# Optimization experiments

Measured on AMD Instinct MI355X. Metric: run time of the kernel, lower is better.

## Reference

```python
import jax, jax.numpy as jnp
import numpy as np

NTRIAL, NNEUR, NT, NT_FULL, NTAU, NLAT, NPAD = 8, 100, 256, 300, 50, 8, 44
LR, JITTER, ZERO_THRESH = 0.2, 1e-3, 1e-5


def setup_inputs() -> dict:
    key = jax.random.key(0)
    k1, k2, k3, k4 = jax.random.split(key, 4)
    Y = jax.random.uniform(k1, (NTRIAL, NNEUR, NT), dtype=jnp.float32)
    raw_input = jax.random.uniform(k2, (NTRIAL, NNEUR, NT_FULL), dtype=jnp.float32)
    kernel = 0.05 * jax.random.normal(k3, (NNEUR, NTAU, NNEUR), dtype=jnp.float32)
    readout = 0.02 * jax.random.normal(k4, (NNEUR, NLAT), dtype=jnp.float32)
    t = jnp.arange(NT, dtype=jnp.float32)
    K = jnp.exp(-(t[:, None] - t[None, :]) ** 2 / (2.0 * 20.0 ** 2))  # RBF latent covariance
    bias = jnp.zeros((), jnp.float32)
    return {"Y": Y, "raw_input": raw_input, "kernel": kernel, "readout": readout,
            "K": K, "bias": bias, "max_iter": 5}


def _conv(raw_input, kernel, npadding):
    # raw_input: (m, i, nt_full); kernel: (i, ntau, j)
    ntrial, ni, nt = raw_input.shape
    zero_pad = jnp.zeros((kernel.shape[0], 1, kernel.shape[2]), kernel.dtype)
    kernel = jnp.concatenate([zero_pad, kernel], axis=1)  # enforce causality
    ntau = kernel.shape[1]
    nn = nt + ntau - 1
    Fx = jnp.fft.fft(raw_input, n=nn, axis=2)[:, :, :, None]   # (m, i, nn, 1)
    Fk = jnp.fft.fft(kernel, n=nn, axis=1)[None]                # (1, i, nn, j)
    G = jnp.fft.ifft(Fx * Fk, axis=2).real
    G = jnp.where(jnp.abs(G) < ZERO_THRESH, 0.0, G)
    G = G[:, :, npadding:nt, :]                                 # (m, i, t, j)
    return jnp.transpose(G, (0, 1, 3, 2)).astype(raw_input.dtype)  # (m, i, j, t)


def _gpfa_poisson_fix_weights(Y, weights, K, bias, max_iter):
    # Y: (m, n, t); weights: (m, n, l, t); K: (t, t)
    ntrial, nneuron, nlatent, nt = weights.shape
    I = jnp.eye(nt, dtype=K.dtype)
    inv_K = jnp.linalg.inv(K + JITTER * I)
    w2 = weights ** 2
    mu0 = jnp.zeros((ntrial, nlatent, nt), K.dtype)
    hess0 = jnp.broadcast_to(inv_K, (ntrial, nlatent, nt, nt)) + jnp.zeros((ntrial, nlatent, 1, 1), K.dtype)

    def step(carry, _):
        mu, hessian, _, _ = carry
        log_lambd = jnp.einsum('mnlt,mlt->mnt', weights, mu) + bias
        hinv = jnp.linalg.inv(hessian)                              # (m, l, t, t)
        dhinv = jnp.diagonal(hinv, axis1=-2, axis2=-1)              # (m, l, t)
        lambd = jnp.exp(log_lambd + 0.5 * jnp.einsum('mlt,mnlt->mnt', dhinv, w2))
        iKh = jnp.einsum('tu,mluv->mltv', inv_K, hinv)              # inv_K @ hessian^{-1}
        muK = jnp.einsum('mlt,tu->mlu', mu, inv_K)
        _, logabs = jnp.linalg.slogdet(iKh)
        loss = (jnp.sum(Y * log_lambd) - jnp.sum(lambd)
                - 0.5 * jnp.sum(muK * mu)
                - 0.5 * jnp.sum(jnp.trace(iKh, axis1=-2, axis2=-1))
                + 0.5 * jnp.sum(logabs) - nt)
        grad = jnp.einsum('mnlt,mnt->mlt', weights, Y - lambd) - muK
        w2l = jnp.einsum('mnlt,mnt->mlt', w2, lambd)                # (m, l, t)
        new_h = -inv_K[None, None] - w2l[..., None] * I             # 4D diagonal add
        mu_upd = jnp.linalg.solve(new_h, grad[..., None])[..., 0]
        return (mu - LR * mu_upd, new_h, lambd, loss), None

    carry0 = (mu0, hess0, jnp.zeros_like(Y), jnp.zeros((), K.dtype))
    (mu, hessian, lambd, loss), _ = jax.lax.scan(step, carry0, None, length=max_iter)
    return mu, lambd, loss


def reference(Y, raw_input, kernel, readout, K, bias, max_iter):
    G = _conv(raw_input, kernel, NPAD)                       # (m, i, j, t)
    weights = jnp.einsum('mijt,il->mjlt', G, readout)        # (m, n=j, l, t)
    mu, lambd, loss = _gpfa_poisson_fix_weights(Y, weights, K, bias, max_iter)
    return mu, lambd, loss
```

## Files before the change

kernel.cpp:

```cpp
#include <hip/hip_runtime.h>

#define NTRIAL 8
#define NNEUR 100
#define NTT 256
#define NT_FULL 300
#define NTAU 50
#define NLAT 8
#define NPAD 44
#define LRATE 0.2f
#define JITTER 0.001f
#define NMAT 64
#define NSLOT 136
#define SPITCH 260
#define NBLKF 35360
#define NBLKF4 8840

__device__ __forceinline__ int bslot(int I, int J){ return ((I*(I+1))>>1) + J; }
__device__ __forceinline__ int eidx(int I, int J, int i, int j){
    return bslot(I,J)*SPITCH + i*16 + ((((j>>2) + (i>>2))&3)<<2) + (j&3);
}
__device__ __forceinline__ int f4idx(int I, int J, int i, int q){
    return bslot(I,J)*65 + i*4 + ((q + (i>>2))&3);
}
__device__ __forceinline__ int bsidx(int J, int k, int col){
    return J*260 + k*16 + ((((col>>2) + (k>>2))&3)<<2) + (col&3);
}
#define DOT4(u,v) (u.x*v.x + u.y*v.y + u.z*v.z + u.w*v.w)

__device__ __forceinline__ void gemm16(const float4* P4, int baseA, int baseB,
                                       int ti, int tj, float acc[4][4]){
    #pragma unroll
    for (int kc = 0; kc < 4; ++kc){
        float4 a0 = P4[baseA + (ti+0)*4 + ((kc + ((ti+0)>>2))&3)];
        float4 a1 = P4[baseA + (ti+1)*4 + ((kc + ((ti+1)>>2))&3)];
        float4 a2 = P4[baseA + (ti+2)*4 + ((kc + ((ti+2)>>2))&3)];
        float4 a3 = P4[baseA + (ti+3)*4 + ((kc + ((ti+3)>>2))&3)];
        float4 b0 = P4[baseB + (tj+0)*4 + ((kc + ((tj+0)>>2))&3)];
        float4 b1 = P4[baseB + (tj+1)*4 + ((kc + ((tj+1)>>2))&3)];
        float4 b2 = P4[baseB + (tj+2)*4 + ((kc + ((tj+2)>>2))&3)];
        float4 b3 = P4[baseB + (tj+3)*4 + ((kc + ((tj+3)>>2))&3)];
        acc[0][0]+=DOT4(a0,b0); acc[0][1]+=DOT4(a0,b1); acc[0][2]+=DOT4(a0,b2); acc[0][3]+=DOT4(a0,b3);
        acc[1][0]+=DOT4(a1,b0); acc[1][1]+=DOT4(a1,b1); acc[1][2]+=DOT4(a1,b2); acc[1][3]+=DOT4(a1,b3);
        acc[2][0]+=DOT4(a2,b0); acc[2][1]+=DOT4(a2,b1); acc[2][2]+=DOT4(a2,b2); acc[2][3]+=DOT4(a2,b3);
        acc[3][0]+=DOT4(a3,b0); acc[3][1]+=DOT4(a3,b1); acc[3][2]+=DOT4(a3,b2); acc[3][3]+=DOT4(a3,b3);
    }
}

__global__ void k_zero(float* mu, float* scal){
    int i = blockIdx.x*256 + threadIdx.x;
    if (i < 16384) mu[i] = 0.f;
    if (i < 64) scal[i] = 0.f;
}

__global__ void k_transpose(const float* __restrict__ kern, float* __restrict__ kt){
    int idx = blockIdx.x*256 + threadIdx.x;
    if (idx >= NNEUR*NTAU*NNEUR) return;
    int i = idx/(NTAU*NNEUR); int rem = idx%(NTAU*NNEUR);
    int tau = rem/NNEUR; int j = rem%NNEUR;
    kt[((size_t)i*NNEUR + j)*NTAU + tau] = kern[idx];
}

__global__ __launch_bounds__(256) void k_conv_weights(const float* __restrict__ raw,
                                                      const float* __restrict__ kt,
                                                      const float* __restrict__ readout,
                                                      float* __restrict__ W){
    int b = blockIdx.x; int m = b / NNEUR; int j = b % NNEUR; int t = threadIdx.x;
    __shared__ float ro[NNEUR*NLAT];
    __shared__ float raw_s[10][NT_FULL];
    __shared__ float kern_s[10][NTAU];
    for (int idx = t; idx < NNEUR*NLAT; idx += 256) ro[idx] = readout[idx];
    float acc[NLAT];
    #pragma unroll
    for (int l = 0; l < NLAT; ++l) acc[l] = 0.f;
    int tmax = min(NTAU, t + NPAD);
    for (int c = 0; c < 10; ++c){
        __syncthreads();
        for (int idx = t; idx < 10*NT_FULL; idx += 256){
            int ii = idx / NT_FULL, tt = idx % NT_FULL;
            raw_s[ii][tt] = raw[((size_t)m*NNEUR + c*10 + ii)*NT_FULL + tt];
        }
        for (int idx = t; idx < 10*NTAU; idx += 256){
            int ii = idx / NTAU, tau = idx % NTAU;
            kern_s[ii][tau] = kt[((size_t)(c*10 + ii)*NNEUR + j)*NTAU + tau];
        }
        __syncthreads();
        for (int ii = 0; ii < 10; ++ii){
            float g = 0.f;
            const float* kr = kern_s[ii];
            const float* rr = raw_s[ii];
            for (int tau = 1; tau <= tmax; ++tau) g += kr[tau-1] * rr[t + NPAD - tau];
            if (fabsf(g) < 1e-5f) g = 0.f;
            const float* rop = &ro[(c*10 + ii)*NLAT];
            #pragma unroll
            for (int l = 0; l < NLAT; ++l) acc[l] += rop[l]*g;
        }
    }
    #pragma unroll
    for (int l = 0; l < NLAT; ++l) W[(((size_t)b)*NLAT + l)*NTT + t] = acc[l];
}

template<int MODE>
__global__ __launch_bounds__(512) void k_fact(
    const float* __restrict__ Kin,
    const float* __restrict__ invKb,
    const float* __restrict__ W,
    const float* __restrict__ Y,
    const float* __restrict__ bias_p,
    const float* __restrict__ muIn,
    const float* __restrict__ diagIn,
    float* __restrict__ muOut,
    float* __restrict__ diagOut,
    float* __restrict__ lambd,
    float* __restrict__ Sout,
    float* __restrict__ scal,
    int it0, int it4, int itSlot)
{
    __shared__ float4 P4[NBLKF4];
    __shared__ float4 Bs4[1040];
    __shared__ float dlog[256];
    __shared__ float idg[16];
    __shared__ float extra[1024];
    float* P    = (float*)P4;
    float* Bsf  = (float*)Bs4;
    float* gs   = extra;
    float* w2ls = extra + 256;
    float* red  = extra + 512;
    float* muown = dlog;
    const int t = threadIdx.x;
    const int b = blockIdx.x;
    const int g = t>>4, gt = t&15;
    const int ti = (gt>>2)<<2, tj = (gt&3)<<2;
    const int lanebase = t & 48;

    if (MODE == 0){
        if (t < 256){
            int r = t, I = r>>4, i = r&15;
            for (int c = 0; c <= r; ++c)
                P[eidx(I, c>>4, i, c&15)] = Kin[r*256 + c] + ((c==r)?JITTER:0.f);
        }
        __syncthreads();
    } else {
        const int m_ = b >> 3, l_ = b & 7;
        const float4* G4 = (const float4*)invKb;
        for (int e = t; e < NBLKF4; e += 512) P4[e] = G4[e];
        const int t2 = t & 255, half = t >> 8;
        float mul[NLAT], dhl[NLAT];
        #pragma unroll
        for (int l = 0; l < NLAT; ++l){
            mul[l] = muIn[((size_t)(m_*NLAT + l))*NTT + t2];
            dhl[l] = it0 ? (1.0f + JITTER) : (-diagIn[((size_t)(m_*NLAT + l))*NTT + t2]);
        }
        if (t < 256) muown[t] = mul[l_];
        float bias = bias_p[0];
        float gacc = 0.f, w2acc = 0.f, yl = 0.f, ls = 0.f;
        for (int n = half*50; n < half*50 + 50; ++n){
            size_t base = (((size_t)(m_*NNEUR + n))*NLAT)*NTT + t2;
            float wl[NLAT];
            float ll = bias, q = 0.f;
            #pragma unroll
            for (int l = 0; l < NLAT; ++l){
                float w = W[base + (size_t)l*NTT];
                wl[l] = w;
                ll += w * mul[l];
                q  += w * w * dhl[l];
            }
            float lam = expf(ll + 0.5f*q);
            float yv = Y[((size_t)(m_*NNEUR + n))*NTT + t2];
            float wo = wl[l_];
            gacc  += wo * (yv - lam);
            w2acc += wo * wo * lam;
            if (it4){
                lambd[((size_t)(m_*NNEUR + n))*NTT + t2] = lam;
                yl += yv * ll; ls += lam;
            }
        }
        Bsf[half*256 + t2]       = gacc;
        Bsf[512 + half*256 + t2] = w2acc;
        __syncthreads();
        if (it4){
            red[t] = yl;
            __syncthreads();
            for (int s = 256; s > 0; s >>= 1){ if (t < s) red[t] += red[t+s]; __syncthreads(); }
            if (t == 0 && l_ == 0) atomicAdd(&scal[0], red[0]);
            __syncthreads();
            red[t] = ls;
            __syncthreads();
            for (int s = 256; s > 0; s >>= 1){ if (t < s) red[t] += red[t+s]; __syncthreads(); }
            if (t == 0 && l_ == 0) atomicAdd(&scal[1], red[0]);
            __syncthreads();
        }
        if (t < 256){
            float gg = Bsf[t] + Bsf[256 + t];
            float w2 = Bsf[512 + t] + Bsf[768 + t];
            int T = t>>4, tb = t&15;
            float mk = 0.f;
            for (int U = 0; U < 16; ++U){
                if (U <= T){
                    #pragma unroll
                    for (int u = 0; u < 16; ++u) mk += muown[U*16+u] * P[eidx(T,U,tb,u)];
                } else {
                    #pragma unroll
                    for (int u = 0; u < 16; ++u) mk += muown[U*16+u] * P[eidx(U,T,u,tb)];
                }
            }
            gs[t]   = gg - mk;
            w2ls[t] = w2;
            red[t]  = mk * muown[t];
        } else red[t] = 0.f;
        if (it4){
            __syncthreads();
            for (int s = 256; s > 0; s >>= 1){ if (t < s) red[t] += red[t+s]; __syncthreads(); }
            if (t == 0) atomicAdd(&scal[2], red[0]);
        }
        __syncthreads();
        if (t < 256) P[eidx(t>>4, t>>4, t&15, t&15)] += w2ls[t];
        __syncthreads();
    }

    for (int p = 0; p < 16; ++p){
        const int pm = p - 1;
        if (g == 31){
            float x[16];
            if (p > 0){
                float acc[4][4];
                #pragma unroll
                for (int aa=0;aa<4;++aa){acc[aa][0]=0;acc[aa][1]=0;acc[aa][2]=0;acc[aa][3]=0;}
                gemm16(P4, bslot(p,pm)*65, bslot(p,pm)*65, ti, tj, acc);
                #pragma unroll
                for (int aa = 0; aa < 4; ++aa){
                    int oi = f4idx(p,p,ti+aa,tj>>2);
                    float4 c = P4[oi];
                    c.x-=acc[aa][0]; c.y-=acc[aa][1]; c.z-=acc[aa][2]; c.w-=acc[aa][3];
                    P4[oi] = c;
                }
            }
            #pragma unroll
            for (int q = 0; q < 4; ++q){
                float4 v = P4[f4idx(p,p,gt,q)];
                x[4*q]=v.x; x[4*q+1]=v.y; x[4*q+2]=v.z; x[4*q+3]=v.w;
            }
            const int i = gt;
            #pragma unroll
            for (int k = 0; k < 16; ++k){
                float piv = __shfl(x[k], lanebase + k, 64);
                float d = sqrtf(piv);
                float dinv = 1.f/d;
                float lik = (i == k) ? d : x[k]*dinv;
                if (i >= k) x[k] = lik;
                #pragma unroll
                for (int c = k+1; c < 16; ++c){
                    float lck = __shfl(x[k], lanebase + c, 64);
                    if (i >= c) x[c] -= lik*lck;
                }
                if (i == k){ idg[k] = dinv; dlog[p*16+k] = d; }
            }
            #pragma unroll
            for (int q = 0; q < 4; ++q)
                P4[f4idx(p,p,i,q)] = make_float4(x[4*q],x[4*q+1],x[4*q+2],x[4*q+3]);
        } else if (p > 0 && g < 28){
            int m = 16 - p;
            int npairs = (m*(m+1))>>1;
            for (int q = 1+g; q < npairs; q += 28){
                int di = (int)floorf((sqrtf(8.f*(float)q + 1.f) - 1.f)*0.5f);
                while (((di+1)*(di+2))>>1 <= q) ++di;
                while ((di*(di+1))>>1 > q) --di;
                int dj = q - ((di*(di+1))>>1);
                int I = p+di, J = p+dj;
                float acc[4][4];
                #pragma unroll
                for (int aa=0;aa<4;++aa){acc[aa][0]=0;acc[aa][1]=0;acc[aa][2]=0;acc[aa][3]=0;}
                gemm16(P4, bslot(I,pm)*65, bslot(J,pm)*65, ti, tj, acc);
                #pragma unroll
                for (int aa = 0; aa < 4; ++aa){
                    int oi = f4idx(I,J,ti+aa,tj>>2);
                    float4 c = P4[oi];
                    c.x-=acc[aa][0]; c.y-=acc[aa][1]; c.z-=acc[aa][2]; c.w-=acc[aa][3];
                    P4[oi] = c;
                }
            }
        }
        __syncthreads();
        if (p < 15){
            int nrows = (15 - p)*16;
            if (t < nrows){
                int r = (p+1)*16 + t;
                int I = r>>4, i = r&15;
                float x[16];
                #pragma unroll
                for (int q = 0; q < 4; ++q){
                    float4 v = P4[f4idx(I,p,i,q)];
                    x[4*q]=v.x; x[4*q+1]=v.y; x[4*q+2]=v.z; x[4*q+3]=v.w;
                }
                #pragma unroll
                for (int c = 0; c < 16; ++c){
                    float s = x[c];
                    #pragma unroll
                    for (int j = 0; j < c; ++j) s -= x[j]*P[eidx(p,p,c,j)];
                    x[c] = s*idg[c];
                }
                #pragma unroll
                for (int q = 0; q < 4; ++q)
                    P4[f4idx(I,p,i,q)] = make_float4(x[4*q],x[4*q+1],x[4*q+2],x[4*q+3]);
            }
        }
        __syncthreads();
    }

    for (int I = 0; I < 16; ++I){
        if (g == 31){
            const int j = gt;
            float col[16];
            #pragma unroll
            for (int k=0;k<16;++k) col[k] = 0.f;
            #pragma unroll
            for (int i = 0; i < 16; ++i){
                float Lii = P[eidx(I,I,i,i)];
                float s = 0.f;
                #pragma unroll
                for (int k = 0; k < 16; ++k){
                    if (k < i){ float term = P[eidx(I,I,i,k)]*col[k]; s += (k >= j) ? term : 0.f; }
                }
                col[i] = (i == j) ? (1.f/Lii) : ((i > j) ? (-s/Lii) : 0.f);
            }
            #pragma unroll
            for (int q = 0; q < 4; ++q)
                P4[f4idx(I,I,j,q)] = make_float4(col[4*q],col[4*q+1],col[4*q+2],col[4*q+3]);
        } else {
            int pj = g>>1, half = g&1;
            if (pj < I){
                const int J = pj;
                float acc[4][4];
                #pragma unroll
                for (int aa=0;aa<4;++aa){acc[aa][0]=0;acc[aa][1]=0;acc[aa][2]=0;acc[aa][3]=0;}
                for (int K = J+half; K < I; K += 2)
                    gemm16(P4, bslot(I,K)*65, bslot(K,J)*65, ti, tj, acc);
                #pragma unroll
                for (int aa = 0; aa < 4; ++aa){
                    #pragma unroll
                    for (int bb = 0; bb < 4; ++bb)
                        acc[aa][bb] += __shfl_xor(acc[aa][bb], 16, 64);
                }
                if (half == 0){
                    #pragma unroll
                    for (int aa = 0; aa < 4; ++aa)
                        Bs4[J*65 + (ti+aa)*4 + (((tj>>2)+((ti+aa)>>2))&3)] =
                            make_float4(acc[aa][0],acc[aa][1],acc[aa][2],acc[aa][3]);
                }
            }
        }
        __syncthreads();
        {
            int pj = g>>1;
            if (pj < I && g < 31){
                const int J = pj;
                const int u = ((g&1)<<4) | gt;
                const int ti2 = ((u>>3)&3)<<2;
                const int tjb = (u&7)<<1;
                float acc2[4][2];
                acc2[0][0]=0;acc2[0][1]=0;acc2[1][0]=0;acc2[1][1]=0;
                acc2[2][0]=0;acc2[2][1]=0;acc2[3][0]=0;acc2[3][1]=0;
                #pragma unroll
                for (int k = 0; k < 16; ++k){
                    float4 sa = P4[f4idx(I,I,k,ti2>>2)];
                    float b0 = Bsf[bsidx(J,k,tjb)];
                    float b1 = Bsf[bsidx(J,k,tjb+1)];
                    acc2[0][0]+=sa.x*b0; acc2[0][1]+=sa.x*b1;
                    acc2[1][0]+=sa.y*b0; acc2[1][1]+=sa.y*b1;
                    acc2[2][0]+=sa.z*b0; acc2[2][1]+=sa.z*b1;
                    acc2[3][0]+=sa.w*b0; acc2[3][1]+=sa.w*b1;
                }
                #pragma unroll
                for (int bb = 0; bb < 2; ++bb)
                    P4[f4idx(I,J,tjb+bb,ti2>>2)] =
                        make_float4(-acc2[0][bb],-acc2[1][bb],-acc2[2][bb],-acc2[3][bb]);
            }
        }
        __syncthreads();
    }

    if (MODE == 0){
        red[t] = (t < 256) ? 2.f*logf(dlog[t]) : 0.f;
        __syncthreads();
        for (int s = 256; s > 0; s >>= 1){ if (t < s) red[t] += red[t+s]; __syncthreads(); }
        if (t == 0) scal[20] = red[0];
        float4* SO = (float4*)Sout;
        for (int e = t; e < NBLKF4; e += 512) SO[e] = P4[e];
        return;
    } else {
        float* zp = Bsf;
        float dsum = 0.f;
        if (t < 256){
            const int J0 = t>>4, j0 = t&15;
            for (int I = J0; I < 16; ++I){
                #pragma unroll
                for (int q = 0; q < 4; ++q){
                    float4 v = P4[f4idx(I,J0,j0,q)];
                    dsum += v.x*v.x + v.y*v.y + v.z*v.z + v.w*v.w;
                }
            }
            diagOut[b*256 + t] = dsum;
            const int Ir = t>>4, rb = t&15;
            float z = 0.f;
            for (int J = 0; J <= Ir; ++J){
                #pragma unroll
                for (int j = 0; j < 16; ++j) z += P[eidx(Ir,J,j,rb)]*gs[J*16+j];
            }
            zp[t] = z;
        }
        __syncthreads();
        if (t < 256){
            const int J0 = t>>4, j0 = t&15;
            float u = 0.f;
            for (int I = J0; I < 16; ++I){
                #pragma unroll
                for (int q = 0; q < 4; ++q){
                    float4 v = P4[f4idx(I,J0,j0,q)];
                    const float* zz = &zp[I*16 + 4*q];
                    u += v.x*zz[0] + v.y*zz[1] + v.z*zz[2] + v.w*zz[3];
                }
            }
            muOut[b*256 + t] = muIn[b*256 + t] + LRATE*u;
            red[t]       = w2ls[t]*dsum;
            red[256 + t] = 2.f*logf(dlog[t]);
        }
        __syncthreads();
        for (int s = 128; s > 0; s >>= 1){
            if (t < s){ red[t] += red[t+s]; red[256+t] += red[256+t+s]; }
            __syncthreads();
        }
        if (t == 0){
            atomicAdd(&scal[8 + itSlot],  red[0] - 256.f);
            atomicAdd(&scal[24 + itSlot], -scal[20] - red[256]);
        }
    }
}

__global__ __launch_bounds__(256) void k_syrk(const float* __restrict__ S,
                                              float* __restrict__ invKb){
    int sidx = blockIdx.x;
    int I = (int)floorf((sqrtf(8.f*(float)sidx + 1.f) - 1.f)*0.5f);
    while (((I+1)*(I+2))>>1 <= sidx) ++I;
    while ((I*(I+1))>>1 > sidx) --I;
    int J = sidx - ((I*(I+1))>>1);
    int t = threadIdx.x; int i = t>>4, j = t&15;
    __shared__ float4 sA[64], sB[64];
    const float4* S4 = (const float4*)S;
    float s = 0.f;
    for (int R = I; R < 16; ++R){
        __syncthreads();
        if (t < 64) sA[t] = S4[bslot(R,I)*65 + t];
        else if (t < 128) sB[t-64] = S4[bslot(R,J)*65 + t-64];
        __syncthreads();
        #pragma unroll
        for (int q = 0; q < 4; ++q){
            float4 a = sA[i*4 + ((q + (i>>2))&3)];
            float4 c = sB[j*4 + ((q + (j>>2))&3)];
            s += a.x*c.x + a.y*c.y + a.z*c.z + a.w*c.w;
        }
    }
    invKb[eidx(I,J,i,j)] = s;
}

__global__ void k_loss(const float* __restrict__ scal, float* __restrict__ out_loss){
    out_loss[0] = scal[0] - scal[1] - 0.5f*scal[2] - 0.5f*scal[8+3] + 0.5f*scal[24+3] - 256.f;
}

__global__ void k_gather(const float* __restrict__ mu, const float* __restrict__ lambd, float* __restrict__ out){
    int idx = blockIdx.x*256 + threadIdx.x;
    if (idx < 16384) out[idx] = mu[idx];
    else if (idx < 16384 + 204800) out[idx] = lambd[idx - 16384];
}

extern "C" void kernel_launch(void* const* d_in, const int* in_sizes, int n_in,
                              void* d_out, int out_size, void* d_ws, size_t ws_size,
                              hipStream_t stream){
    (void)in_sizes; (void)n_in; (void)out_size; (void)ws_size;
    const float* Y       = (const float*)d_in[0];
    const float* raw     = (const float*)d_in[1];
    const float* kern    = (const float*)d_in[2];
    const float* readout = (const float*)d_in[3];
    const float* K       = (const float*)d_in[4];
    const float* bias    = (const float*)d_in[5];
    float* out = (float*)d_out;
    float* ws  = (float*)d_ws;

    float* invKb  = ws;
    float* Sblk   = invKb + NBLKF;
    float* W      = Sblk + NBLKF;
    float* muA    = W + 1638400;
    float* muB    = muA + 16384;
    float* lambd  = muB + 16384;
    float* diagA  = lambd + 204800;
    float* diagB  = diagA + 16384;
    float* scal   = diagB + 16384;
    float* kt     = scal + 64;

    k_zero<<<64, 256, 0, stream>>>(muA, scal);
    k_transpose<<<(NNEUR*NTAU*NNEUR + 255)/256, 256, 0, stream>>>(kern, kt);
    k_conv_weights<<<NTRIAL*NNEUR, 256, 0, stream>>>(raw, kt, readout, W);

    k_fact<0><<<1, 512, 0, stream>>>(K, nullptr, nullptr, nullptr, nullptr, nullptr, nullptr,
                                     nullptr, nullptr, nullptr, Sblk, scal, 0, 0, 0);
    k_syrk<<<NSLOT, 256, 0, stream>>>(Sblk, invKb);

    for (int it = 0; it < 5; ++it){
        const float* muI = (it & 1) ? muB : muA;
        float*       muO = (it & 1) ? muA : muB;
        const float* dI  = (it & 1) ? diagB : diagA;
        float*       dO  = (it & 1) ? diagA : diagB;
        k_fact<1><<<NMAT, 512, 0, stream>>>(nullptr, invKb, W, Y, bias, muI, dI,
                                            muO, dO, lambd, nullptr, scal,
                                            (it == 0) ? 1 : 0, (it == 4) ? 1 : 0, it);
    }
    k_loss<<<1, 1, 0, stream>>>(scal, out + 16384 + 204800);
    k_gather<<<864, 256, 0, stream>>>(muB, lambd, out);
}
```

Before: 1.537 ms.

## Split gradient into separate kernel and fuse Cholesky inversion into factorization loop

Moves the Poisson rate/gradient computation out of the factorization kernel into a new k_grad2 kernel. Each block of k_grad2 handles a slice of neurons and produces all 8 latents for one trial, so W is read once per trial instead of eight times. The blocked Cholesky is also restructured so each diagonal block is inverted right after it is factored. The panel solve and the L-inverse off-diagonal products become small GEMMs against the inverted diagonal block, interleaved in one pass instead of a separate second sweep. This adds a kernel launch and global partial buffers per iteration, and changes the accumulation order.

```diff
diff --git a/kernel.cpp b/kernel.cpp
--- a/kernel.cpp
+++ b/kernel.cpp
@@ -16,29 +16,30 @@
 #define NBLKF4 8840
 
 __device__ __forceinline__ int bslot(int I, int J){ return ((I*(I+1))>>1) + J; }
+__device__ __forceinline__ int rcs(int i, int j){
+    return i*16 + ((((j>>2) + (i>>2))&3)<<2) + (j&3);
+}
 __device__ __forceinline__ int eidx(int I, int J, int i, int j){
-    return bslot(I,J)*SPITCH + i*16 + ((((j>>2) + (i>>2))&3)<<2) + (j&3);
-}
+    return bslot(I,J)*SPITCH + rcs(i,j);
+}
+__device__ __forceinline__ int rc4(int i, int q){ return i*4 + ((q + (i>>2))&3); }
 __device__ __forceinline__ int f4idx(int I, int J, int i, int q){
-    return bslot(I,J)*65 + i*4 + ((q + (i>>2))&3);
-}
-__device__ __forceinline__ int bsidx(int J, int k, int col){
-    return J*260 + k*16 + ((((col>>2) + (k>>2))&3)<<2) + (col&3);
+    return bslot(I,J)*65 + rc4(i,q);
 }
 #define DOT4(u,v) (u.x*v.x + u.y*v.y + u.z*v.z + u.w*v.w)
 
-__device__ __forceinline__ void gemm16(const float4* P4, int baseA, int baseB,
+__device__ __forceinline__ void gemmRR(const float4* A, int baseA, const float4* B, int baseB,
                                        int ti, int tj, float acc[4][4]){
     #pragma unroll
     for (int kc = 0; kc < 4; ++kc){
-        float4 a0 = P4[baseA + (ti+0)*4 + ((kc + ((ti+0)>>2))&3)];
-        float4 a1 = P4[baseA + (ti+1)*4 + ((kc + ((ti+1)>>2))&3)];
-        float4 a2 = P4[baseA + (ti+2)*4 + ((kc + ((ti+2)>>2))&3)];
-        float4 a3 = P4[baseA + (ti+3)*4 + ((kc + ((ti+3)>>2))&3)];
-        float4 b0 = P4[baseB + (tj+0)*4 + ((kc + ((tj+0)>>2))&3)];
-        float4 b1 = P4[baseB + (tj+1)*4 + ((kc + ((tj+1)>>2))&3)];
-        float4 b2 = P4[baseB + (tj+2)*4 + ((kc + ((tj+2)>>2))&3)];
-        float4 b3 = P4[baseB + (tj+3)*4 + ((kc + ((tj+3)>>2))&3)];
+        float4 a0 = A[baseA + rc4(ti+0,kc)];
+        float4 a1 = A[baseA + rc4(ti+1,kc)];
+        float4 a2 = A[baseA + rc4(ti+2,kc)];
+        float4 a3 = A[baseA + rc4(ti+3,kc)];
+        float4 b0 = B[baseB + rc4(tj+0,kc)];
+        float4 b1 = B[baseB + rc4(tj+1,kc)];
+        float4 b2 = B[baseB + rc4(tj+2,kc)];
+        float4 b3 = B[baseB + rc4(tj+3,kc)];
         acc[0][0]+=DOT4(a0,b0); acc[0][1]+=DOT4(a0,b1); acc[0][2]+=DOT4(a0,b2); acc[0][3]+=DOT4(a0,b3);
         acc[1][0]+=DOT4(a1,b0); acc[1][1]+=DOT4(a1,b1); acc[1][2]+=DOT4(a1,b2); acc[1][3]+=DOT4(a1,b3);
         acc[2][0]+=DOT4(a2,b0); acc[2][1]+=DOT4(a2,b1); acc[2][2]+=DOT4(a2,b2); acc[2][3]+=DOT4(a2,b3);
@@ -99,32 +100,86 @@
     for (int l = 0; l < NLAT; ++l) W[(((size_t)b)*NLAT + l)*NTT + t] = acc[l];
 }
 
+__global__ __launch_bounds__(256) void k_grad2(const float* __restrict__ W, const float* __restrict__ Y,
+                                               const float* __restrict__ bias_p,
+                                               const float* __restrict__ muIn, const float* __restrict__ diagIn,
+                                               float* __restrict__ gradPart, float* __restrict__ w2lPart,
+                                               float* __restrict__ lambd, float* __restrict__ scal,
+                                               int it0, int it4){
+    int blk = blockIdx.x; int m = blk >> 3; int chunk = blk & 7;
+    int n0 = chunk*12 + (chunk < 4 ? chunk : 4);
+    int cnt = 12 + (chunk < 4 ? 1 : 0);
+    int t = threadIdx.x;
+    __shared__ float r1[256], r2[256];
+    float mul[NLAT], dhl[NLAT];
+    #pragma unroll
+    for (int l = 0; l < NLAT; ++l){
+        mul[l] = muIn[((size_t)(m*NLAT + l))*NTT + t];
+        dhl[l] = it0 ? (1.0f + JITTER) : (-diagIn[((size_t)(m*NLAT + l))*NTT + t]);
+    }
+    float bias = bias_p[0];
+    float ga[NLAT], wa[NLAT];
+    #pragma unroll
+    for (int l = 0; l < NLAT; ++l){ ga[l] = 0.f; wa[l] = 0.f; }
+    float yl = 0.f, ls = 0.f;
+    for (int n = n0; n < n0 + cnt; ++n){
+        size_t base = (((size_t)(m*NNEUR + n))*NLAT)*NTT + t;
+        float wl[NLAT];
+        float ll = bias, q = 0.f;
+        #pragma unroll
+        for (int l = 0; l < NLAT; ++l){
+            float w = W[base + (size_t)l*NTT];
+            wl[l] = w;
+            ll += w * mul[l];
+            q  += w * w * dhl[l];
+        }
+        float lam = expf(ll + 0.5f*q);
+        float yv = Y[((size_t)(m*NNEUR + n))*NTT + t];
+        float d = yv - lam;
+        #pragma unroll
+        for (int l = 0; l < NLAT; ++l){ ga[l] += wl[l]*d; wa[l] += wl[l]*wl[l]*lam; }
+        if (it4){
+            lambd[((size_t)(m*NNEUR + n))*NTT + t] = lam;
+            yl += yv * ll; ls += lam;
+        }
+    }
+    #pragma unroll
+    for (int l = 0; l < NLAT; ++l){
+        gradPart[((size_t)((chunk<<6) + m*NLAT + l))*NTT + t] = ga[l];
+        w2lPart [((size_t)((chunk<<6) + m*NLAT + l))*NTT + t] = wa[l];
+    }
+    if (it4){
+        r1[t] = yl; r2[t] = ls;
+        __syncthreads();
+        for (int s = 128; s > 0; s >>= 1){ if (t < s){ r1[t]+=r1[t+s]; r2[t]+=r2[t+s]; } __syncthreads(); }
+        if (t == 0){ atomicAdd(&scal[0], r1[0]); atomicAdd(&scal[1], r2[0]); }
+    }
+}
+
 template<int MODE>
 __global__ __launch_bounds__(512) void k_fact(
     const float* __restrict__ Kin,
     const float* __restrict__ invKb,
-    const float* __restrict__ W,
-    const float* __restrict__ Y,
-    const float* __restrict__ bias_p,
+    const float* __restrict__ gradPart,
+    const float* __restrict__ w2lPart,
     const float* __restrict__ muIn,
-    const float* __restrict__ diagIn,
     float* __restrict__ muOut,
     float* __restrict__ diagOut,
-    float* __restrict__ lambd,
     float* __restrict__ Sout,
     float* __restrict__ scal,
-    int it0, int it4, int itSlot)
+    int it4, int itSlot)
 {
     __shared__ float4 P4[NBLKF4];
-    __shared__ float4 Bs4[1040];
+    __shared__ float4 Bs4[1104];
+    __shared__ float4 XinvL4[130];
     __shared__ float dlog[256];
     __shared__ float idg[16];
-    __shared__ float extra[1024];
-    float* P    = (float*)P4;
-    float* Bsf  = (float*)Bs4;
-    float* gs   = extra;
-    float* w2ls = extra + 256;
-    float* red  = extra + 512;
+    float* P     = (float*)P4;
+    float* Bsf   = (float*)Bs4;
+    float* gs    = Bsf + 3900;
+    float* w2ls  = Bsf + 4156;
+    float* red   = Bsf;
+    float* zp    = Bsf + 512;
     float* muown = dlog;
     const int t = threadIdx.x;
     const int b = blockIdx.x;
@@ -140,58 +195,17 @@
         }
         __syncthreads();
     } else {
-        const int m_ = b >> 3, l_ = b & 7;
         const float4* G4 = (const float4*)invKb;
         for (int e = t; e < NBLKF4; e += 512) P4[e] = G4[e];
-        const int t2 = t & 255, half = t >> 8;
-        float mul[NLAT], dhl[NLAT];
-        #pragma unroll
-        for (int l = 0; l < NLAT; ++l){
-            mul[l] = muIn[((size_t)(m_*NLAT + l))*NTT + t2];
-            dhl[l] = it0 ? (1.0f + JITTER) : (-diagIn[((size_t)(m_*NLAT + l))*NTT + t2]);
-        }
-        if (t < 256) muown[t] = mul[l_];
-        float bias = bias_p[0];
-        float gacc = 0.f, w2acc = 0.f, yl = 0.f, ls = 0.f;
-        for (int n = half*50; n < half*50 + 50; ++n){
-            size_t base = (((size_t)(m_*NNEUR + n))*NLAT)*NTT + t2;
-            float wl[NLAT];
-            float ll = bias, q = 0.f;
+        if (t < 256) muown[t] = muIn[(size_t)b*NTT + t];
+        __syncthreads();
+        if (t < 256){
+            float gg = 0.f, ww = 0.f;
             #pragma unroll
-            for (int l = 0; l < NLAT; ++l){
-                float w = W[base + (size_t)l*NTT];
-                wl[l] = w;
-                ll += w * mul[l];
-                q  += w * w * dhl[l];
-            }
-            float lam = expf(ll + 0.5f*q);
-            float yv = Y[((size_t)(m_*NNEUR + n))*NTT + t2];
-            float wo = wl[l_];
-            gacc  += wo * (yv - lam);
-            w2acc += wo * wo * lam;
-            if (it4){
-                lambd[((size_t)(m_*NNEUR + n))*NTT + t2] = lam;
-                yl += yv * ll; ls += lam;
-            }
-        }
-        Bsf[half*256 + t2]       = gacc;
-        Bsf[512 + half*256 + t2] = w2acc;
-        __syncthreads();
-        if (it4){
-            red[t] = yl;
-            __syncthreads();
-            for (int s = 256; s > 0; s >>= 1){ if (t < s) red[t] += red[t+s]; __syncthreads(); }
-            if (t == 0 && l_ == 0) atomicAdd(&scal[0], red[0]);
-            __syncthreads();
-            red[t] = ls;
-            __syncthreads();
-            for (int s = 256; s > 0; s >>= 1){ if (t < s) red[t] += red[t+s]; __syncthreads(); }
-            if (t == 0 && l_ == 0) atomicAdd(&scal[1], red[0]);
-            __syncthreads();
-        }
-        if (t < 256){
-            float gg = Bsf[t] + Bsf[256 + t];
-            float w2 = Bsf[512 + t] + Bsf[768 + t];
+            for (int c = 0; c < 8; ++c){
+                gg += gradPart[((size_t)((c<<6) + b))*NTT + t];
+                ww += w2lPart [((size_t)((c<<6) + b))*NTT + t];
+            }
             int T = t>>4, tb = t&15;
             float mk = 0.f;
             for (int U = 0; U < 16; ++U){
@@ -204,12 +218,12 @@
                 }
             }
             gs[t]   = gg - mk;
-            w2ls[t] = w2;
+            w2ls[t] = ww;
             red[t]  = mk * muown[t];
-        } else red[t] = 0.f;
+        }
         if (it4){
             __syncthreads();
-            for (int s = 256; s > 0; s >>= 1){ if (t < s) red[t] += red[t+s]; __syncthreads(); }
+            for (int s = 128; s > 0; s >>= 1){ if (t < s) red[t] += red[t+s]; __syncthreads(); }
             if (t == 0) atomicAdd(&scal[2], red[0]);
         }
         __syncthreads();
@@ -217,162 +231,135 @@
         __syncthreads();
     }
 
-    for (int p = 0; p < 16; ++p){
-        const int pm = p - 1;
+    for (int p = 0; p <= 16; ++p){
+        const int r = p - 1;
         if (g == 31){
-            float x[16];
-            if (p > 0){
+            if (p < 16){
+                float x[16];
+                if (p > 0){
+                    float acc[4][4];
+                    #pragma unroll
+                    for (int aa=0;aa<4;++aa){acc[aa][0]=0;acc[aa][1]=0;acc[aa][2]=0;acc[aa][3]=0;}
+                    gemmRR(P4, bslot(p,r)*65, P4, bslot(p,r)*65, ti, tj, acc);
+                    #pragma unroll
+                    for (int aa = 0; aa < 4; ++aa){
+                        int oi = f4idx(p,p,ti+aa,tj>>2);
+                        float4 c = P4[oi];
+                        c.x-=acc[aa][0]; c.y-=acc[aa][1]; c.z-=acc[aa][2]; c.w-=acc[aa][3];
+                        P4[oi] = c;
+                    }
+                }
+                #pragma unroll
+                for (int q = 0; q < 4; ++q){
+                    float4 v = P4[f4idx(p,p,gt,q)];
+                    x[4*q]=v.x; x[4*q+1]=v.y; x[4*q+2]=v.z; x[4*q+3]=v.w;
+                }
+                const int i = gt;
+                #pragma unroll
+                for (int k = 0; k < 16; ++k){
+                    float piv = __shfl(x[k], lanebase + k, 64);
+                    float d = sqrtf(piv);
+                    float dinv = 1.f/d;
+                    float lik = (i == k) ? d : x[k]*dinv;
+                    if (i >= k) x[k] = lik;
+                    #pragma unroll
+                    for (int c = k+1; c < 16; ++c){
+                        float lck = __shfl(x[k], lanebase + c, 64);
+                        if (i >= c) x[c] -= lik*lck;
+                    }
+                    if (i == k){ idg[k] = dinv; dlog[p*16+k] = d; }
+                }
+                float col[16];
+                #pragma unroll
+                for (int ii = 0; ii < 16; ++ii){
+                    float s = 0.f;
+                    #pragma unroll
+                    for (int k = 0; k < 16; ++k){
+                        if (k < ii){
+                            float lik = __shfl(x[k], lanebase + ii, 64);
+                            s += lik * col[k];
+                        }
+                    }
+                    float v = ((gt == ii) ? 1.f : -s) * idg[ii];
+                    col[ii] = (gt <= ii) ? v : 0.f;
+                }
+                #pragma unroll
+                for (int q = 0; q < 4; ++q)
+                    P4[f4idx(p,p,gt,q)] = make_float4(col[4*q],col[4*q+1],col[4*q+2],col[4*q+3]);
+                float* XL = (float*)(XinvL4 + (p&1)*65);
+                #pragma unroll
+                for (int ii = 0; ii < 16; ++ii) XL[rcs(ii, gt)] = col[ii];
+            }
+        } else {
+            int m16 = 16 - p;
+            int ntrail = (p >= 1 && p < 16) ? ((m16*(m16+1))>>1) - 1 : 0;
+            int nsm = (p >= 1) ? (p - 1) : 0;
+            for (int id = g; id < ntrail + nsm; id += 31){
+                if (id < ntrail){
+                    int q = id + 1;
+                    int di = (int)floorf((sqrtf(8.f*(float)q + 1.f) - 1.f)*0.5f);
+                    while (((di+1)*(di+2))>>1 <= q) ++di;
+                    while ((di*(di+1))>>1 > q) --di;
+                    int dj = q - ((di*(di+1))>>1);
+                    int I = p + di, J = p + dj;
+                    float acc[4][4];
+                    #pragma unroll
+                    for (int aa=0;aa<4;++aa){acc[aa][0]=0;acc[aa][1]=0;acc[aa][2]=0;acc[aa][3]=0;}
+                    gemmRR(P4, bslot(I,r)*65, P4, bslot(J,r)*65, ti, tj, acc);
+                    #pragma unroll
+                    for (int aa = 0; aa < 4; ++aa){
+                        int oi = f4idx(I,J,ti+aa,tj>>2);
+                        float4 c = P4[oi];
+                        c.x-=acc[aa][0]; c.y-=acc[aa][1]; c.z-=acc[aa][2]; c.w-=acc[aa][3];
+                        P4[oi] = c;
+                    }
+                } else {
+                    int J = id - ntrail;
+                    float acc[4][4];
+                    #pragma unroll
+                    for (int aa=0;aa<4;++aa){acc[aa][0]=0;acc[aa][1]=0;acc[aa][2]=0;acc[aa][3]=0;}
+                    gemmRR(Bs4, J*65, XinvL4, (r&1)*65, ti, tj, acc);
+                    #pragma unroll
+                    for (int aa = 0; aa < 4; ++aa)
+                        P4[f4idx(r,J,ti+aa,tj>>2)] =
+                            make_float4(-acc[aa][0],-acc[aa][1],-acc[aa][2],-acc[aa][3]);
+                }
+            }
+        }
+        __syncthreads();
+        if (p == 16) break;
+        if (g < 2*p){
+            int J = g>>1, half = g&1;
+            float acc[4][4];
+            #pragma unroll
+            for (int aa=0;aa<4;++aa){acc[aa][0]=0;acc[aa][1]=0;acc[aa][2]=0;acc[aa][3]=0;}
+            for (int K = J + half; K < p; K += 2)
+                gemmRR(P4, bslot(p,K)*65, P4, bslot(K,J)*65, ti, tj, acc);
+            #pragma unroll
+            for (int aa = 0; aa < 4; ++aa){
+                #pragma unroll
+                for (int bb = 0; bb < 4; ++bb)
+                    acc[aa][bb] += __shfl_xor(acc[aa][bb], 16, 64);
+            }
+            if (half == 0){
+                float* BJ = Bsf + J*260;
+                #pragma unroll
+                for (int aa = 0; aa < 4; ++aa)
+                    #pragma unroll
+                    for (int bb = 0; bb < 4; ++bb)
+                        BJ[rcs(tj+bb, ti+aa)] = acc[aa][bb];
+            }
+        } else {
+            int I = p + 1 + (g - 2*p);
+            if (I < 16){
                 float acc[4][4];
                 #pragma unroll
                 for (int aa=0;aa<4;++aa){acc[aa][0]=0;acc[aa][1]=0;acc[aa][2]=0;acc[aa][3]=0;}
-                gemm16(P4, bslot(p,pm)*65, bslot(p,pm)*65, ti, tj, acc);
-                #pragma unroll
-                for (int aa = 0; aa < 4; ++aa){
-                    int oi = f4idx(p,p,ti+aa,tj>>2);
-                    float4 c = P4[oi];
-                    c.x-=acc[aa][0]; c.y-=acc[aa][1]; c.z-=acc[aa][2]; c.w-=acc[aa][3];
-                    P4[oi] = c;
-                }
-            }
-            #pragma unroll
-            for (int q = 0; q < 4; ++q){
-                float4 v = P4[f4idx(p,p,gt,q)];
-                x[4*q]=v.x; x[4*q+1]=v.y; x[4*q+2]=v.z; x[4*q+3]=v.w;
-            }
-            const int i = gt;
-            #pragma unroll
-            for (int k = 0; k < 16; ++k){
-                float piv = __shfl(x[k], lanebase + k, 64);
-                float d = sqrtf(piv);
-                float dinv = 1.f/d;
-                float lik = (i == k) ? d : x[k]*dinv;
-                if (i >= k) x[k] = lik;
-                #pragma unroll
-                for (int c = k+1; c < 16; ++c){
-                    float lck = __shfl(x[k], lanebase + c, 64);
-                    if (i >= c) x[c] -= lik*lck;
-                }
-                if (i == k){ idg[k] = dinv; dlog[p*16+k] = d; }
-            }
-            #pragma unroll
-            for (int q = 0; q < 4; ++q)
-                P4[f4idx(p,p,i,q)] = make_float4(x[4*q],x[4*q+1],x[4*q+2],x[4*q+3]);
-        } else if (p > 0 && g < 28){
-            int m = 16 - p;
-            int npairs = (m*(m+1))>>1;
-            for (int q = 1+g; q < npairs; q += 28){
-                int di = (int)floorf((sqrtf(8.f*(float)q + 1.f) - 1.f)*0.5f);
-                while (((di+1)*(di+2))>>1 <= q) ++di;
-                while ((di*(di+1))>>1 > q) --di;
-                int dj = q - ((di*(di+1))>>1);
-                int I = p+di, J = p+dj;
-                float acc[4][4];
-                #pragma unroll
-                for (int aa=0;aa<4;++aa){acc[aa][0]=0;acc[aa][1]=0;acc[aa][2]=0;acc[aa][3]=0;}
-                gemm16(P4, bslot(I,pm)*65, bslot(J,pm)*65, ti, tj, acc);
-                #pragma unroll
-                for (int aa = 0; aa < 4; ++aa){
-                    int oi = f4idx(I,J,ti+aa,tj>>2);
-                    float4 c = P4[oi];
-                    c.x-=acc[aa][0]; c.y-=acc[aa][1]; c.z-=acc[aa][2]; c.w-=acc[aa][3];
-                    P4[oi] = c;
-                }
-            }
-        }
-        __syncthreads();
-        if (p < 15){
-            int nrows = (15 - p)*16;
-            if (t < nrows){
-                int r = (p+1)*16 + t;
-                int I = r>>4, i = r&15;
-                float x[16];
-                #pragma unroll
-                for (int q = 0; q < 4; ++q){
-                    float4 v = P4[f4idx(I,p,i,q)];
-                    x[4*q]=v.x; x[4*q+1]=v.y; x[4*q+2]=v.z; x[4*q+3]=v.w;
-                }
-                #pragma unroll
-                for (int c = 0; c < 16; ++c){
-                    float s = x[c];
-                    #pragma unroll
-                    for (int j = 0; j < c; ++j) s -= x[j]*P[eidx(p,p,c,j)];
-                    x[c] = s*idg[c];
-                }
-                #pragma unroll
-                for (int q = 0; q < 4; ++q)
-                    P4[f4idx(I,p,i,q)] = make_float4(x[4*q],x[4*q+1],x[4*q+2],x[4*q+3]);
-            }
-        }
-        __syncthreads();
-    }
-
-    for (int I = 0; I < 16; ++I){
-        if (g == 31){
-            const int j = gt;
-            float col[16];
-            #pragma unroll
-            for (int k=0;k<16;++k) col[k] = 0.f;
-            #pragma unroll
-            for (int i = 0; i < 16; ++i){
-                float Lii = P[eidx(I,I,i,i)];
-                float s = 0.f;
-                #pragma unroll
-                for (int k = 0; k < 16; ++k){
-                    if (k < i){ float term = P[eidx(I,I,i,k)]*col[k]; s += (k >= j) ? term : 0.f; }
-                }
-                col[i] = (i == j) ? (1.f/Lii) : ((i > j) ? (-s/Lii) : 0.f);
-            }
-            #pragma unroll
-            for (int q = 0; q < 4; ++q)
-                P4[f4idx(I,I,j,q)] = make_float4(col[4*q],col[4*q+1],col[4*q+2],col[4*q+3]);
-        } else {
-            int pj = g>>1, half = g&1;
-            if (pj < I){
-                const int J = pj;
-                float acc[4][4];
-                #pragma unroll
-                for (int aa=0;aa<4;++aa){acc[aa][0]=0;acc[aa][1]=0;acc[aa][2]=0;acc[aa][3]=0;}
-                for (int K = J+half; K < I; K += 2)
-                    gemm16(P4, bslot(I,K)*65, bslot(K,J)*65, ti, tj, acc);
-                #pragma unroll
-                for (int aa = 0; aa < 4; ++aa){
-                    #pragma unroll
-                    for (int bb = 0; bb < 4; ++bb)
-                        acc[aa][bb] += __shfl_xor(acc[aa][bb], 16, 64);
-                }
-                if (half == 0){
-                    #pragma unroll
-                    for (int aa = 0; aa < 4; ++aa)
-                        Bs4[J*65 + (ti+aa)*4 + (((tj>>2)+((ti+aa)>>2))&3)] =
-                            make_float4(acc[aa][0],acc[aa][1],acc[aa][2],acc[aa][3]);
-                }
-            }
-        }
-        __syncthreads();
-        {
-            int pj = g>>1;
-            if (pj < I && g < 31){
-                const int J = pj;
-                const int u = ((g&1)<<4) | gt;
-                const int ti2 = ((u>>3)&3)<<2;
-                const int tjb = (u&7)<<1;
-                float acc2[4][2];
-                acc2[0][0]=0;acc2[0][1]=0;acc2[1][0]=0;acc2[1][1]=0;
-                acc2[2][0]=0;acc2[2][1]=0;acc2[3][0]=0;acc2[3][1]=0;
-                #pragma unroll
-                for (int k = 0; k < 16; ++k){
-                    float4 sa = P4[f4idx(I,I,k,ti2>>2)];
-                    float b0 = Bsf[bsidx(J,k,tjb)];
-                    float b1 = Bsf[bsidx(J,k,tjb+1)];
-                    acc2[0][0]+=sa.x*b0; acc2[0][1]+=sa.x*b1;
-                    acc2[1][0]+=sa.y*b0; acc2[1][1]+=sa.y*b1;
-                    acc2[2][0]+=sa.z*b0; acc2[2][1]+=sa.z*b1;
-                    acc2[3][0]+=sa.w*b0; acc2[3][1]+=sa.w*b1;
-                }
-                #pragma unroll
-                for (int bb = 0; bb < 2; ++bb)
-                    P4[f4idx(I,J,tjb+bb,ti2>>2)] =
-                        make_float4(-acc2[0][bb],-acc2[1][bb],-acc2[2][bb],-acc2[3][bb]);
+                gemmRR(P4, bslot(I,p)*65, XinvL4, (p&1)*65, ti, tj, acc);
+                #pragma unroll
+                for (int aa = 0; aa < 4; ++aa)
+                    P4[f4idx(I,p,ti+aa,tj>>2)] =
+                        make_float4(acc[aa][0],acc[aa][1],acc[aa][2],acc[aa][3]);
             }
         }
         __syncthreads();
@@ -381,13 +368,12 @@
     if (MODE == 0){
         red[t] = (t < 256) ? 2.f*logf(dlog[t]) : 0.f;
         __syncthreads();
-        for (int s = 256; s > 0; s >>= 1){ if (t < s) red[t] += red[t+s]; __syncthreads(); }
+        for (int s = 128; s > 0; s >>= 1){ if (t < s) red[t] += red[t+s]; __syncthreads(); }
         if (t == 0) scal[20] = red[0];
         float4* SO = (float4*)Sout;
         for (int e = t; e < NBLKF4; e += 512) SO[e] = P4[e];
         return;
     } else {
-        float* zp = Bsf;
         float dsum = 0.f;
         if (t < 256){
             const int J0 = t>>4, j0 = t&15;
@@ -398,7 +384,7 @@
                     dsum += v.x*v.x + v.y*v.y + v.z*v.z + v.w*v.w;
                 }
             }
-            diagOut[b*256 + t] = dsum;
+            diagOut[(size_t)b*NTT + t] = dsum;
             const int Ir = t>>4, rb = t&15;
             float z = 0.f;
             for (int J = 0; J <= Ir; ++J){
@@ -419,7 +405,7 @@
                     u += v.x*zz[0] + v.y*zz[1] + v.z*zz[2] + v.w*zz[3];
                 }
             }
-            muOut[b*256 + t] = muIn[b*256 + t] + LRATE*u;
+            muOut[(size_t)b*NTT + t] = muIn[(size_t)b*NTT + t] + LRATE*u;
             red[t]       = w2ls[t]*dsum;
             red[256 + t] = 2.f*logf(dlog[t]);
         }
@@ -453,8 +439,8 @@
         __syncthreads();
         #pragma unroll
         for (int q = 0; q < 4; ++q){
-            float4 a = sA[i*4 + ((q + (i>>2))&3)];
-            float4 c = sB[j*4 + ((q + (j>>2))&3)];
+            float4 a = sA[rc4(i,q)];
+            float4 c = sB[rc4(j,q)];
             s += a.x*c.x + a.y*c.y + a.z*c.z + a.w*c.w;
         }
     }
@@ -484,23 +470,25 @@
     float* out = (float*)d_out;
     float* ws  = (float*)d_ws;
 
-    float* invKb  = ws;
-    float* Sblk   = invKb + NBLKF;
-    float* W      = Sblk + NBLKF;
-    float* muA    = W + 1638400;
-    float* muB    = muA + 16384;
-    float* lambd  = muB + 16384;
-    float* diagA  = lambd + 204800;
-    float* diagB  = diagA + 16384;
-    float* scal   = diagB + 16384;
-    float* kt     = scal + 64;
+    float* invKb    = ws;
+    float* Sblk     = invKb + NBLKF;
+    float* W        = Sblk + NBLKF;
+    float* muA      = W + 1638400;
+    float* muB      = muA + 16384;
+    float* lambd    = muB + 16384;
+    float* diagA    = lambd + 204800;
+    float* diagB    = diagA + 16384;
+    float* gradPart = diagB + 16384;
+    float* w2lPart  = gradPart + 131072;
+    float* scal     = w2lPart + 131072;
+    float* kt       = scal + 64;
 
     k_zero<<<64, 256, 0, stream>>>(muA, scal);
     k_transpose<<<(NNEUR*NTAU*NNEUR + 255)/256, 256, 0, stream>>>(kern, kt);
     k_conv_weights<<<NTRIAL*NNEUR, 256, 0, stream>>>(raw, kt, readout, W);
 
-    k_fact<0><<<1, 512, 0, stream>>>(K, nullptr, nullptr, nullptr, nullptr, nullptr, nullptr,
-                                     nullptr, nullptr, nullptr, Sblk, scal, 0, 0, 0);
+    k_fact<0><<<1, 512, 0, stream>>>(K, nullptr, nullptr, nullptr, nullptr,
+                                     nullptr, nullptr, Sblk, scal, 0, 0);
     k_syrk<<<NSLOT, 256, 0, stream>>>(Sblk, invKb);
 
     for (int it = 0; it < 5; ++it){
@@ -508,9 +496,12 @@
         float*       muO = (it & 1) ? muA : muB;
         const float* dI  = (it & 1) ? diagB : diagA;
         float*       dO  = (it & 1) ? diagA : diagB;
-        k_fact<1><<<NMAT, 512, 0, stream>>>(nullptr, invKb, W, Y, bias, muI, dI,
-                                            muO, dO, lambd, nullptr, scal,
-                                            (it == 0) ? 1 : 0, (it == 4) ? 1 : 0, it);
+        int it0 = (it == 0) ? 1 : 0;
+        int it4 = (it == 4) ? 1 : 0;
+        k_grad2<<<64, 256, 0, stream>>>(W, Y, bias, muI, dI, gradPart, w2lPart,
+                                        lambd, scal, it0, it4);
+        k_fact<1><<<NMAT, 512, 0, stream>>>(nullptr, invKb, gradPart, w2lPart, muI,
+                                            muO, dO, nullptr, scal, it4, it);
     }
     k_loss<<<1, 1, 0, stream>>>(scal, out + 16384 + 204800);
     k_gather<<<864, 256, 0, stream>>>(muB, lambd, out);
```

Measured after the change: 1.695 ms. 10.3% more time.
